# Performance work log

Hardware: AMD Instinct MI355X
Metric: run time of the kernel (lower is better)

The kernel has to match this reference:

```python
import jax, jax.numpy as jnp
import numpy as np
from jax import lax

NMS_THRESH = 0.5      # IoU threshold 'thresh' in the torch forward
MAX_PROPOSALS = 1000  # 'max_proposals' in the torch forward


def setup_inputs() -> dict:
    key = jax.random.key(0)
    k1, k2, k3 = jax.random.split(key, 3)
    N = 10000
    # realistic xyxy boxes inside a ~1000x1000 image
    centers = jax.random.uniform(k1, (N, 2), dtype=jnp.float32) * 1000.0
    wh = jax.random.uniform(k2, (N, 2), dtype=jnp.float32) * 99.0 + 1.0
    boxes = jnp.concatenate([centers - wh / 2.0, centers + wh / 2.0], axis=-1)  # [N,4]
    scores = jax.random.uniform(k3, (N,), dtype=jnp.float32)  # [N]
    return {"boxes": boxes, "scores": scores}


def _pairwise_iou(b):
    # b: [N,4] xyxy, sorted by score. Returns [N,N] IoU matrix.
    x1, y1, x2, y2 = b[:, 0], b[:, 1], b[:, 2], b[:, 3]
    areas = (x2 - x1) * (y2 - y1)                      # [N]
    ix1 = jnp.maximum(x1[:, None], x1[None, :])
    iy1 = jnp.maximum(y1[:, None], y1[None, :])
    ix2 = jnp.minimum(x2[:, None], x2[None, :])
    iy2 = jnp.minimum(y2[:, None], y2[None, :])
    iw = jnp.maximum(ix2 - ix1, 0.0)
    ih = jnp.maximum(iy2 - iy1, 0.0)
    inter = iw * ih                                    # [N,N]
    union = areas[:, None] + areas[None, :] - inter
    return inter / jnp.maximum(union, 1e-9)


def reference(boxes, scores):
    # Faithful greedy NMS: sort by score desc, suppress lower-scored boxes
    # with IoU > thresh against any kept higher-scored box.
    N = boxes.shape[0]
    order = jnp.argsort(-scores)
    b = boxes[order]        # [N,4] score-sorted
    s = scores[order]       # [N]
    ious = _pairwise_iou(b)  # [N,N]
    idx = jnp.arange(N)

    def body(i, keep):
        # if box i is still kept, suppress all later boxes overlapping it
        suppress = keep[i] & (ious[i] > NMS_THRESH) & (idx > i)
        return keep & ~suppress

    keep = lax.fori_loop(0, N, body, jnp.ones((N,), dtype=bool))
    # keep = keep[:max_proposals] in the torch code: first MAX_PROPOSALS kept boxes
    rank = jnp.cumsum(keep.astype(jnp.int32)) - 1
    keep = keep & (rank < MAX_PROPOSALS)
    # fixed-shape equivalent of boxlist[keep]: zero out suppressed entries
    boxes_out = jnp.where(keep[:, None], b, 0.0)   # [N,4]
    scores_out = jnp.where(keep, s, 0.0)           # [N]
    return boxes_out, scores_out, keep
```

## Files before the change

kernel.cpp:

```cpp
#include <hip/hip_runtime.h>
#include <stdint.h>

#define MAX_PROPOSALS 1000
#define WPAD 160
#define NSTRIPE 128
#define SCAP 2048
#define LDSE 13312
#define G 10
#define NCELL (G * G)
#define NB 4096

__device__ __forceinline__ int cell_of(float lo, float hi) {
  int g = (int)((lo + hi) * 0.005f);
  return min(max(g, 0), G - 1);
}
__device__ __forceinline__ int bucket_of(float s) {
  int b = (int)(s * (float)NB);
  return min(max(b, 0), NB - 1);
}

__global__ __launch_bounds__(1024) void k_zero(int* __restrict__ p, int n) {
  for (int i = threadIdx.x; i < n; i += 1024) p[i] = 0;
}

__global__ __launch_bounds__(256) void k_hist(const float* __restrict__ scores,
                                              const float4* __restrict__ boxes,
                                              int* __restrict__ hist,
                                              int* __restrict__ cellCnt, int N) {
  int i = blockIdx.x * 256 + threadIdx.x;
  if (i >= N) return;
  float s = scores[i];
  atomicAdd(&hist[bucket_of(s)], 1);
  float4 b = boxes[i];
  int cell = cell_of(b.y, b.w) * G + cell_of(b.x, b.z);
  atomicAdd(&cellCnt[cell], 1);
}

__global__ __launch_bounds__(1024) void k_prefix(const int* __restrict__ hist,
                       int* __restrict__ bstart, int* __restrict__ bcur,
                       const int* __restrict__ cellCnt,
                       int* __restrict__ cellStart, int* __restrict__ cellCur) {
  __shared__ int wsum[16];
  int tid = threadIdx.x, l = tid & 63, wv = tid >> 6;
  int h[4];
  int base4 = tid * 4;
  int s = 0;
  #pragma unroll
  for (int k = 0; k < 4; ++k) { h[k] = hist[base4 + k]; s += h[k]; }
  int inc = s;
  #pragma unroll
  for (int d = 1; d < 64; d <<= 1) {
    int v = __shfl_up(inc, d, 64);
    if (l >= d) inc += v;
  }
  if (l == 63) wsum[wv] = inc;
  __syncthreads();
  if (tid == 0) {
    int run = 0;
    for (int w = 0; w < 16; ++w) { int v = wsum[w]; wsum[w] = run; run += v; }
  }
  __syncthreads();
  int ex = wsum[wv] + inc - s;
  #pragma unroll
  for (int k = 0; k < 4; ++k) { bstart[base4 + k] = ex; bcur[base4 + k] = ex; ex += h[k]; }
  if (tid == 1023) bstart[NB] = ex;

  if (wv == 0) {
    int a = (2 * l < NCELL) ? cellCnt[2 * l] : 0;
    int b = (2 * l + 1 < NCELL) ? cellCnt[2 * l + 1] : 0;
    int s2 = a + b, inc2 = s2;
    #pragma unroll
    for (int d = 1; d < 64; d <<= 1) {
      int v = __shfl_up(inc2, d, 64);
      if (l >= d) inc2 += v;
    }
    int ex2 = inc2 - s2;
    if (2 * l < NCELL)     { cellStart[2 * l] = ex2;         cellCur[2 * l] = ex2; }
    if (2 * l + 1 < NCELL) { cellStart[2 * l + 1] = ex2 + a; cellCur[2 * l + 1] = ex2 + a; }
    if (l == 63) cellStart[NCELL] = inc2;
  }
}

__global__ __launch_bounds__(256) void k_bscatter(const float* __restrict__ scores,
                       int* __restrict__ bcur, uint64_t* __restrict__ bkey,
                       int* __restrict__ bidx, int N) {
  int i = blockIdx.x * 256 + threadIdx.x;
  if (i >= N) return;
  float s = scores[i];
  uint64_t key = ((uint64_t)__float_as_uint(s) << 32) | (uint64_t)(0xFFFFFFFFu - (uint32_t)i);
  int b = bucket_of(s);
  int pos = atomicAdd(&bcur[b], 1);
  bkey[pos] = key;
  bidx[pos] = i;
}

__global__ __launch_bounds__(256) void k_rankscatter(const uint64_t* __restrict__ bkey,
                       const int* __restrict__ bidx, const int* __restrict__ bstart,
                       const float4* __restrict__ boxes,
                       int* __restrict__ cellCur,
                       float4* __restrict__ sbox, float* __restrict__ ss,
                       float4* __restrict__ sboxC, int* __restrict__ cellRank, int N) {
  int p = blockIdx.x * 256 + threadIdx.x;
  if (p >= N) return;
  uint64_t key = bkey[p];
  float s = __uint_as_float((uint32_t)(key >> 32));
  int b = bucket_of(s);
  int q0 = bstart[b], q1 = bstart[b + 1];
  int r = N - q1;
  for (int q = q0; q < q1; ++q) r += (bkey[q] > key);
  int idx = bidx[p];
  float4 bx = boxes[idx];
  sbox[r] = bx;
  ss[r] = s;
  int cell = cell_of(bx.y, bx.w) * G + cell_of(bx.x, bx.z);
  int cpos = atomicAdd(&cellCur[cell], 1);
  sboxC[cpos] = bx;
  cellRank[cpos] = r;
}

__global__ __launch_bounds__(256) void k_maskR2(const float4* __restrict__ sbox,
                        const int* __restrict__ cellStart,
                        const float4* __restrict__ sboxC, const int* __restrict__ cellRank,
                        uint32_t* __restrict__ edges, int* __restrict__ ecnt, int N) {
  int wv = threadIdx.x >> 6, lane = threadIdx.x & 63;
  int i = blockIdx.x * 4 + wv;
  if (i >= N) return;
  int stripe = blockIdx.x & (NSTRIPE - 1);
  uint32_t* estr = edges + (size_t)stripe * SCAP;

  float4 iB = sbox[i];
  float iar = (iB.z - iB.x) * (iB.w - iB.y);
  int cx = cell_of(iB.x, iB.z), cy = cell_of(iB.y, iB.w);
  int x0 = max(cx - 1, 0), x1 = min(cx + 1, G - 1);
  int y0 = max(cy - 1, 0), y1 = min(cy + 1, G - 1);

  for (int ry = y0; ry <= y1; ++ry) {
    int s = cellStart[ry * G + x0];
    int e = cellStart[ry * G + x1 + 1];
    if (s >= e) continue;

    int p = s + lane;
    int pc = (p < e) ? p : s;
    float4 cB = sboxC[pc];
    int rk = cellRank[pc];

    for (int p0 = s; p0 < e; p0 += 64) {
      float4 curB = cB;
      int currk = rk;
      bool curv = (p0 + lane) < e;

      if (p0 + 64 < e) {
        int np = p0 + 64 + lane;
        int npc = (np < e) ? np : s;
        cB = sboxC[npc];
        rk = cellRank[npc];
      }

      float car = (curB.z - curB.x) * (curB.w - curB.y);
      float ix1 = fmaxf(iB.x, curB.x);
      float iy1 = fmaxf(iB.y, curB.y);
      float ix2 = fminf(iB.z, curB.z);
      float iy2 = fminf(iB.w, curB.w);
      float iw = fmaxf(ix2 - ix1, 0.0f);
      float ih = fmaxf(iy2 - iy1, 0.0f);
      float inter = iw * ih;
      float uni = (iar + car) - inter;
      float m_ = fmaxf(uni, 1e-9f);
      float t_ = 0.5f * m_;
      bool pred = (inter > t_) && curv && (currk > i);
      bool ambig = pred && (inter <= t_ + t_ * 3e-7f);
      if (__builtin_expect(__ballot(ambig) != 0ull, 0)) {
        if (ambig) pred = (inter / m_) > 0.5f;
      }
      uint64_t ball = __ballot(pred);
      if (__builtin_expect(ball != 0ull, 0)) {
        int cnt = __popcll(ball);
        int base = 0;
        if (lane == 0) base = atomicAdd(&ecnt[stripe], cnt);
        base = __shfl(base, 0, 64);
        if (pred) {
          int pos = base + __popcll(ball & ((1ull << lane) - 1ull));
          if (pos < SCAP) estr[pos] = ((uint32_t)i << 14) | (uint32_t)currk;
        }
      }
    }
  }
}

__global__ __launch_bounds__(1024) void k_scanJ(const uint32_t* __restrict__ edges,
                                                const int* __restrict__ ecnt,
                                                uint64_t* __restrict__ keepw,
                                                int* __restrict__ wpref, int N) {
  const int tid = threadIdx.x, l = tid & 63, wave = tid >> 6;
  const int nw = (N + 63) >> 6;
  const int nh = 2 * nw;

  __shared__ uint32_t eL[LDSE];
  __shared__ int scnt[NSTRIPE], soff[NSTRIPE];
  __shared__ int eTot;
  __shared__ uint32_t kc[2 * WPAD];
  __shared__ uint32_t kn[2 * WPAD];
  __shared__ uint32_t baseL[2 * WPAD];
  __shared__ uint64_t keepL[WPAD];
  __shared__ int chgS;

  if (wave == 0) {
    int a = min(ecnt[2 * l], SCAP);
    int b = min(ecnt[2 * l + 1], SCAP);
    int s = a + b, inc = s;
    #pragma unroll
    for (int d = 1; d < 64; d <<= 1) {
      int v = __shfl_up(inc, d, 64);
      if (l >= d) inc += v;
    }
    int ex = inc - s;
    scnt[2 * l] = a;     soff[2 * l] = ex;
    scnt[2 * l + 1] = b; soff[2 * l + 1] = ex + a;
    if (l == 63) eTot = min(inc, LDSE);
  }
  for (int w = tid; w < 2 * WPAD; w += 1024) {
    long lo = (long)(w >> 1) * 64 + (long)(w & 1) * 32;
    long rem = (long)N - lo;
    uint32_t m = (rem >= 32) ? 0xFFFFFFFFu : ((rem <= 0) ? 0u : ((1u << rem) - 1u));
    baseL[w] = m;
    kc[w] = m;
  }
  __syncthreads();

  for (int s = wave; s < NSTRIPE; s += 16) {
    int cnt = scnt[s], off = soff[s];
    const uint32_t* src = edges + (size_t)s * SCAP;
    for (int k = l; k < cnt; k += 64) {
      int dst = off + k;
      if (dst < LDSE) eL[dst] = src[k];
    }
  }
  __syncthreads();
  int EL = eTot;

  for (int round = 0; round < 10001; ++round) {
    for (int w = tid; w < nh; w += 1024) kn[w] = baseL[w];
    if (tid == 0) chgS = 0;
    __syncthreads();

    for (int e = tid; e < EL; e += 1024) {
      uint32_t p = eL[e];
      int i = (int)(p >> 14);
      int j = (int)(p & 0x3FFFu);
      if ((kc[i >> 5] >> (i & 31)) & 1u)
        atomicAnd(&kn[j >> 5], ~(1u << (j & 31)));
    }
    __syncthreads();

    int local = 0;
    for (int w = tid; w < nh; w += 1024) {
      uint32_t a = kn[w];
      if (a != kc[w]) local = 1;
      kc[w] = a;
    }
    if (local) chgS = 1;
    __syncthreads();
    bool done = (chgS == 0);
    __syncthreads();
    if (done) break;
  }

  for (int i = tid; i < WPAD; i += 1024)
    keepL[i] = (i < nw) ? (((uint64_t)kc[2 * i + 1] << 32) | (uint64_t)kc[2 * i]) : 0ull;
  __syncthreads();

  if (wave == 0) {
    uint64_t k0 = keepL[l], k1 = keepL[64 + l];
    uint64_t k2v = (128 + l < WPAD) ? keepL[128 + l] : 0ull;
    int p0 = __popcll(k0), p1 = __popcll(k1), p2 = __popcll(k2v);
    int s0 = p0, s1 = p1, s2 = p2;
    #pragma unroll
    for (int d = 1; d < 64; d <<= 1) {
      int v0 = __shfl_up(s0, d, 64), v1 = __shfl_up(s1, d, 64), v2 = __shfl_up(s2, d, 64);
      if (l >= d) { s0 += v0; s1 += v1; s2 += v2; }
    }
    int tot0 = __shfl(s0, 63, 64);
    int tot1 = __shfl(s1, 63, 64);
    keepw[l] = k0;
    keepw[64 + l] = k1;
    if (128 + l < WPAD) keepw[128 + l] = k2v;
    wpref[l] = s0 - p0;
    wpref[64 + l] = tot0 + s1 - p1;
    if (128 + l < WPAD) wpref[128 + l] = tot0 + tot1 + s2 - p2;
  }
}

__global__ __launch_bounds__(256) void k_out(const float4* __restrict__ sbox,
                      const float* __restrict__ ss,
                      const uint64_t* __restrict__ keepw, const int* __restrict__ wpref,
                      float* __restrict__ out, int N) {
  int i = blockIdx.x * 256 + threadIdx.x;
  if (i >= N) return;
  int w = i >> 6, b = i & 63;
  uint64_t kw = keepw[w];
  bool kept = (kw >> b) & 1ull;
  int rank = wpref[w] + __popcll(kw & ((1ull << b) - 1ull));
  bool fin = kept && (rank < MAX_PROPOSALS);
  float4 bx = sbox[i];
  if (!fin) { bx.x = 0.0f; bx.y = 0.0f; bx.z = 0.0f; bx.w = 0.0f; }
  ((float4*)out)[i] = bx;
  out[(size_t)4 * N + i] = fin ? ss[i] : 0.0f;
  out[(size_t)5 * N + i] = fin ? 1.0f : 0.0f;
}

extern "C" void kernel_launch(void* const* d_in, const int* in_sizes, int n_in,
                              void* d_out, int out_size, void* d_ws, size_t ws_size,
                              hipStream_t stream) {
  const float4* boxes = (const float4*)d_in[0];
  const float* scores = (const float*)d_in[1];
  int N = in_sizes[1];

  char* ws = (char*)d_ws;
  size_t off = 0;
  int* hist    = (int*)(ws + off); off += NB * 4;
  int* ecnt    = (int*)(ws + off); off += NSTRIPE * 4;
  int* cellCnt = (int*)(ws + off); off += NCELL * 4;
  int zints = NB + NSTRIPE + NCELL;
  off = (off + 255) & ~(size_t)255;
  int* bstart   = (int*)(ws + off); off += (NB + 1) * 4;
  int* bcur     = (int*)(ws + off); off += NB * 4;
  int* cellStart= (int*)(ws + off); off += (NCELL + 1) * 4;
  int* cellCur  = (int*)(ws + off); off += NCELL * 4;
  off = (off + 255) & ~(size_t)255;
  uint64_t* bkey = (uint64_t*)(ws + off); off += (size_t)N * 8;
  int* bidx      = (int*)(ws + off); off += (size_t)N * 4;
  off = (off + 255) & ~(size_t)255;
  float4* sbox  = (float4*)(ws + off); off += (size_t)N * 16;
  float4* sboxC = (float4*)(ws + off); off += (size_t)N * 16;
  float* ss     = (float*)(ws + off);  off += (size_t)N * 4;
  int* cellRank = (int*)(ws + off); off += (size_t)N * 4;
  off = (off + 255) & ~(size_t)255;
  uint32_t* edges = (uint32_t*)(ws + off); off += (size_t)NSTRIPE * SCAP * 4;
  uint64_t* keepw = (uint64_t*)(ws + off); off += WPAD * 8;
  int* wpref      = (int*)(ws + off); off += WPAD * 4;

  int nblk = (N + 255) / 256;

  k_zero<<<1, 1024, 0, stream>>>(hist, zints);
  k_hist<<<nblk, 256, 0, stream>>>(scores, boxes, hist, cellCnt, N);
  k_prefix<<<1, 1024, 0, stream>>>(hist, bstart, bcur, cellCnt, cellStart, cellCur);
  k_bscatter<<<nblk, 256, 0, stream>>>(scores, bcur, bkey, bidx, N);
  k_rankscatter<<<nblk, 256, 0, stream>>>(bkey, bidx, bstart, boxes, cellCur,
                                          sbox, ss, sboxC, cellRank, N);
  k_maskR2<<<(N + 3) / 4, 256, 0, stream>>>(sbox, cellStart, sboxC, cellRank, edges, ecnt, N);
  k_scanJ<<<1, 1024, 0, stream>>>(edges, ecnt, keepw, wpref, N);
  k_out<<<nblk, 256, 0, stream>>>(sbox, ss, keepw, wpref, (float*)d_out, N);
}
```

Baseline: 121.6 us.

## Fuse all NMS stages into one cooperative kernel with grid syncs

Replaces eight separate kernel launches with a single cooperative kernel of 256 blocks of 256 threads. Stages are separated by grid.sync() and use grid-stride loops. The goal is to remove per-launch overhead and inter-kernel gaps, which dominate a pipeline of many tiny kernels. The trade-offs: the serial label-propagation stage now runs in one 256-thread block instead of 1024 threads, the mask stage has far fewer waves in flight, and each grid barrier has its own cost.

```diff
diff --git a/kernel.cpp b/kernel.cpp
--- a/kernel.cpp
+++ b/kernel.cpp
@@ -1,5 +1,8 @@
 #include <hip/hip_runtime.h>
+#include <hip/hip_cooperative_groups.h>
 #include <stdint.h>
+
+namespace cg = cooperative_groups;
 
 #define MAX_PROPOSALS 1000
 #define WPAD 160
@@ -9,6 +12,8 @@
 #define G 10
 #define NCELL (G * G)
 #define NB 4096
+#define NBLK 256
+#define NTHR 256
 
 __device__ __forceinline__ int cell_of(float lo, float hi) {
   int g = (int)((lo + hi) * 0.005f);
@@ -19,53 +24,68 @@
   return min(max(b, 0), NB - 1);
 }
 
-__global__ __launch_bounds__(1024) void k_zero(int* __restrict__ p, int n) {
-  for (int i = threadIdx.x; i < n; i += 1024) p[i] = 0;
-}
-
-__global__ __launch_bounds__(256) void k_hist(const float* __restrict__ scores,
-                                              const float4* __restrict__ boxes,
-                                              int* __restrict__ hist,
-                                              int* __restrict__ cellCnt, int N) {
-  int i = blockIdx.x * 256 + threadIdx.x;
-  if (i >= N) return;
-  float s = scores[i];
-  atomicAdd(&hist[bucket_of(s)], 1);
-  float4 b = boxes[i];
-  int cell = cell_of(b.y, b.w) * G + cell_of(b.x, b.z);
-  atomicAdd(&cellCnt[cell], 1);
-}
-
-__global__ __launch_bounds__(1024) void k_prefix(const int* __restrict__ hist,
-                       int* __restrict__ bstart, int* __restrict__ bcur,
-                       const int* __restrict__ cellCnt,
-                       int* __restrict__ cellStart, int* __restrict__ cellCur) {
-  __shared__ int wsum[16];
-  int tid = threadIdx.x, l = tid & 63, wv = tid >> 6;
-  int h[4];
-  int base4 = tid * 4;
-  int s = 0;
-  #pragma unroll
-  for (int k = 0; k < 4; ++k) { h[k] = hist[base4 + k]; s += h[k]; }
-  int inc = s;
-  #pragma unroll
-  for (int d = 1; d < 64; d <<= 1) {
-    int v = __shfl_up(inc, d, 64);
-    if (l >= d) inc += v;
-  }
-  if (l == 63) wsum[wv] = inc;
-  __syncthreads();
-  if (tid == 0) {
-    int run = 0;
-    for (int w = 0; w < 16; ++w) { int v = wsum[w]; wsum[w] = run; run += v; }
-  }
-  __syncthreads();
-  int ex = wsum[wv] + inc - s;
-  #pragma unroll
-  for (int k = 0; k < 4; ++k) { bstart[base4 + k] = ex; bcur[base4 + k] = ex; ex += h[k]; }
-  if (tid == 1023) bstart[NB] = ex;
-
-  if (wv == 0) {
+__global__ __launch_bounds__(NTHR) void k_all(
+    const float4* __restrict__ boxes, const float* __restrict__ scores,
+    int* __restrict__ hist,
+    int* __restrict__ ecnt, int* __restrict__ cellCnt,
+    int* __restrict__ bstart, int* __restrict__ bcur,
+    int* __restrict__ cellStart, int* __restrict__ cellCur,
+    uint64_t* __restrict__ bkey, int* __restrict__ bidx,
+    float4* __restrict__ sbox, float* __restrict__ ss,
+    float4* __restrict__ sboxC, int* __restrict__ cellRank,
+    uint32_t* __restrict__ edges, uint64_t* __restrict__ keepw,
+    int* __restrict__ wpref, float* __restrict__ out, int N) {
+  cg::grid_group grid = cg::this_grid();
+  const int tid = threadIdx.x, bid = blockIdx.x;
+  const int gtid = bid * NTHR + tid;
+  const int P = NBLK * NTHR;
+  const int l = tid & 63, wv = tid >> 6;
+  const int nw = (N + 63) >> 6;
+  const int nh = 2 * nw;
+
+  __shared__ int psum[4];
+  __shared__ uint32_t eL[LDSE];
+  __shared__ int scnt[NSTRIPE], soff[NSTRIPE];
+  __shared__ int eTotS;
+  __shared__ uint32_t kc[2 * WPAD], kn[2 * WPAD], baseL[2 * WPAD];
+  __shared__ uint64_t keepL[WPAD];
+  __shared__ int chgS;
+
+  for (int i = gtid; i < NB + NSTRIPE + NCELL; i += P) hist[i] = 0;
+  grid.sync();
+
+  for (int i = gtid; i < N; i += P) {
+    float s = scores[i];
+    atomicAdd(&hist[bucket_of(s)], 1);
+    float4 b = boxes[i];
+    atomicAdd(&cellCnt[cell_of(b.y, b.w) * G + cell_of(b.x, b.z)], 1);
+  }
+  grid.sync();
+
+  if (bid == 0) {
+    int h[16];
+    int base16 = tid * 16;
+    int s = 0;
+    #pragma unroll
+    for (int k = 0; k < 16; ++k) { h[k] = hist[base16 + k]; s += h[k]; }
+    int inc = s;
+    #pragma unroll
+    for (int d = 1; d < 64; d <<= 1) {
+      int v = __shfl_up(inc, d, 64);
+      if (l >= d) inc += v;
+    }
+    if (l == 63) psum[wv] = inc;
+    __syncthreads();
+    if (tid == 0) {
+      int run = 0;
+      for (int w = 0; w < 4; ++w) { int v = psum[w]; psum[w] = run; run += v; }
+    }
+    __syncthreads();
+    int ex = psum[wv] + inc - s;
+    #pragma unroll
+    for (int k = 0; k < 16; ++k) { bstart[base16 + k] = ex; bcur[base16 + k] = ex; ex += h[k]; }
+    if (tid == NTHR - 1) bstart[NB] = ex;
+  } else if (bid == 1 && wv == 0) {
     int a = (2 * l < NCELL) ? cellCnt[2 * l] : 0;
     int b = (2 * l + 1 < NCELL) ? cellCnt[2 * l + 1] : 0;
     int s2 = a + b, inc2 = s2;
@@ -79,233 +99,191 @@
     if (2 * l + 1 < NCELL) { cellStart[2 * l + 1] = ex2 + a; cellCur[2 * l + 1] = ex2 + a; }
     if (l == 63) cellStart[NCELL] = inc2;
   }
-}
-
-__global__ __launch_bounds__(256) void k_bscatter(const float* __restrict__ scores,
-                       int* __restrict__ bcur, uint64_t* __restrict__ bkey,
-                       int* __restrict__ bidx, int N) {
-  int i = blockIdx.x * 256 + threadIdx.x;
-  if (i >= N) return;
-  float s = scores[i];
-  uint64_t key = ((uint64_t)__float_as_uint(s) << 32) | (uint64_t)(0xFFFFFFFFu - (uint32_t)i);
-  int b = bucket_of(s);
-  int pos = atomicAdd(&bcur[b], 1);
-  bkey[pos] = key;
-  bidx[pos] = i;
-}
-
-__global__ __launch_bounds__(256) void k_rankscatter(const uint64_t* __restrict__ bkey,
-                       const int* __restrict__ bidx, const int* __restrict__ bstart,
-                       const float4* __restrict__ boxes,
-                       int* __restrict__ cellCur,
-                       float4* __restrict__ sbox, float* __restrict__ ss,
-                       float4* __restrict__ sboxC, int* __restrict__ cellRank, int N) {
-  int p = blockIdx.x * 256 + threadIdx.x;
-  if (p >= N) return;
-  uint64_t key = bkey[p];
-  float s = __uint_as_float((uint32_t)(key >> 32));
-  int b = bucket_of(s);
-  int q0 = bstart[b], q1 = bstart[b + 1];
-  int r = N - q1;
-  for (int q = q0; q < q1; ++q) r += (bkey[q] > key);
-  int idx = bidx[p];
-  float4 bx = boxes[idx];
-  sbox[r] = bx;
-  ss[r] = s;
-  int cell = cell_of(bx.y, bx.w) * G + cell_of(bx.x, bx.z);
-  int cpos = atomicAdd(&cellCur[cell], 1);
-  sboxC[cpos] = bx;
-  cellRank[cpos] = r;
-}
-
-__global__ __launch_bounds__(256) void k_maskR2(const float4* __restrict__ sbox,
-                        const int* __restrict__ cellStart,
-                        const float4* __restrict__ sboxC, const int* __restrict__ cellRank,
-                        uint32_t* __restrict__ edges, int* __restrict__ ecnt, int N) {
-  int wv = threadIdx.x >> 6, lane = threadIdx.x & 63;
-  int i = blockIdx.x * 4 + wv;
-  if (i >= N) return;
-  int stripe = blockIdx.x & (NSTRIPE - 1);
-  uint32_t* estr = edges + (size_t)stripe * SCAP;
-
-  float4 iB = sbox[i];
-  float iar = (iB.z - iB.x) * (iB.w - iB.y);
-  int cx = cell_of(iB.x, iB.z), cy = cell_of(iB.y, iB.w);
-  int x0 = max(cx - 1, 0), x1 = min(cx + 1, G - 1);
-  int y0 = max(cy - 1, 0), y1 = min(cy + 1, G - 1);
-
-  for (int ry = y0; ry <= y1; ++ry) {
-    int s = cellStart[ry * G + x0];
-    int e = cellStart[ry * G + x1 + 1];
-    if (s >= e) continue;
-
-    int p = s + lane;
-    int pc = (p < e) ? p : s;
-    float4 cB = sboxC[pc];
-    int rk = cellRank[pc];
-
-    for (int p0 = s; p0 < e; p0 += 64) {
-      float4 curB = cB;
-      int currk = rk;
-      bool curv = (p0 + lane) < e;
-
-      if (p0 + 64 < e) {
-        int np = p0 + 64 + lane;
-        int npc = (np < e) ? np : s;
-        cB = sboxC[npc];
-        rk = cellRank[npc];
-      }
-
-      float car = (curB.z - curB.x) * (curB.w - curB.y);
-      float ix1 = fmaxf(iB.x, curB.x);
-      float iy1 = fmaxf(iB.y, curB.y);
-      float ix2 = fminf(iB.z, curB.z);
-      float iy2 = fminf(iB.w, curB.w);
-      float iw = fmaxf(ix2 - ix1, 0.0f);
-      float ih = fmaxf(iy2 - iy1, 0.0f);
-      float inter = iw * ih;
-      float uni = (iar + car) - inter;
-      float m_ = fmaxf(uni, 1e-9f);
-      float t_ = 0.5f * m_;
-      bool pred = (inter > t_) && curv && (currk > i);
-      bool ambig = pred && (inter <= t_ + t_ * 3e-7f);
-      if (__builtin_expect(__ballot(ambig) != 0ull, 0)) {
-        if (ambig) pred = (inter / m_) > 0.5f;
-      }
-      uint64_t ball = __ballot(pred);
-      if (__builtin_expect(ball != 0ull, 0)) {
-        int cnt = __popcll(ball);
-        int base = 0;
-        if (lane == 0) base = atomicAdd(&ecnt[stripe], cnt);
-        base = __shfl(base, 0, 64);
-        if (pred) {
-          int pos = base + __popcll(ball & ((1ull << lane) - 1ull));
-          if (pos < SCAP) estr[pos] = ((uint32_t)i << 14) | (uint32_t)currk;
+  grid.sync();
+
+  for (int i = gtid; i < N; i += P) {
+    float s = scores[i];
+    uint64_t key = ((uint64_t)__float_as_uint(s) << 32) | (uint64_t)(0xFFFFFFFFu - (uint32_t)i);
+    int pos = atomicAdd(&bcur[bucket_of(s)], 1);
+    bkey[pos] = key;
+    bidx[pos] = i;
+  }
+  grid.sync();
+
+  for (int p = gtid; p < N; p += P) {
+    uint64_t key = bkey[p];
+    float s = __uint_as_float((uint32_t)(key >> 32));
+    int b = bucket_of(s);
+    int q0 = bstart[b], q1 = bstart[b + 1];
+    int r = N - q1;
+    for (int q = q0; q < q1; ++q) r += (bkey[q] > key);
+    float4 bx = boxes[bidx[p]];
+    sbox[r] = bx;
+    ss[r] = s;
+    int cpos = atomicAdd(&cellCur[cell_of(bx.y, bx.w) * G + cell_of(bx.x, bx.z)], 1);
+    sboxC[cpos] = bx;
+    cellRank[cpos] = r;
+  }
+  grid.sync();
+
+  {
+    int wvid = (bid << 2) | wv;
+    for (int i = wvid; i < N; i += NBLK * 4) {
+      int stripe = i & (NSTRIPE - 1);
+      uint32_t* estr = edges + (size_t)stripe * SCAP;
+      float4 iB = sbox[i];
+      float iar = (iB.z - iB.x) * (iB.w - iB.y);
+      int cx = cell_of(iB.x, iB.z), cy = cell_of(iB.y, iB.w);
+      int x0 = max(cx - 1, 0), x1 = min(cx + 1, G - 1);
+      int y0 = max(cy - 1, 0), y1 = min(cy + 1, G - 1);
+
+      for (int ry = y0; ry <= y1; ++ry) {
+        int s = cellStart[ry * G + x0];
+        int e = cellStart[ry * G + x1 + 1];
+        if (s >= e) continue;
+        int p = s + l;
+        int pc = (p < e) ? p : s;
+        float4 cB = sboxC[pc];
+        int rk = cellRank[pc];
+        for (int p0 = s; p0 < e; p0 += 64) {
+          float4 curB = cB;
+          int currk = rk;
+          bool curv = (p0 + l) < e;
+          if (p0 + 64 < e) {
+            int np = p0 + 64 + l;
+            int npc = (np < e) ? np : s;
+            cB = sboxC[npc];
+            rk = cellRank[npc];
+          }
+          float car = (curB.z - curB.x) * (curB.w - curB.y);
+          float ix1 = fmaxf(iB.x, curB.x);
+          float iy1 = fmaxf(iB.y, curB.y);
+          float ix2 = fminf(iB.z, curB.z);
+          float iy2 = fminf(iB.w, curB.w);
+          float iw = fmaxf(ix2 - ix1, 0.0f);
+          float ih = fmaxf(iy2 - iy1, 0.0f);
+          float inter = iw * ih;
+          float uni = (iar + car) - inter;
+          float m_ = fmaxf(uni, 1e-9f);
+          float t_ = 0.5f * m_;
+          bool pred = (inter > t_) && curv && (currk > i);
+          bool ambig = pred && (inter <= t_ + t_ * 3e-7f);
+          if (__builtin_expect(__ballot(ambig) != 0ull, 0)) {
+            if (ambig) pred = (inter / m_) > 0.5f;
+          }
+          uint64_t ball = __ballot(pred);
+          if (__builtin_expect(ball != 0ull, 0)) {
+            int cnt = __popcll(ball);
+            int base = 0;
+            if (l == 0) base = atomicAdd(&ecnt[stripe], cnt);
+            base = __shfl(base, 0, 64);
+            if (pred) {
+              int pos = base + __popcll(ball & ((1ull << l) - 1ull));
+              if (pos < SCAP) estr[pos] = ((uint32_t)i << 14) | (uint32_t)currk;
+            }
+          }
         }
       }
     }
   }
-}
-
-__global__ __launch_bounds__(1024) void k_scanJ(const uint32_t* __restrict__ edges,
-                                                const int* __restrict__ ecnt,
-                                                uint64_t* __restrict__ keepw,
-                                                int* __restrict__ wpref, int N) {
-  const int tid = threadIdx.x, l = tid & 63, wave = tid >> 6;
-  const int nw = (N + 63) >> 6;
-  const int nh = 2 * nw;
-
-  __shared__ uint32_t eL[LDSE];
-  __shared__ int scnt[NSTRIPE], soff[NSTRIPE];
-  __shared__ int eTot;
-  __shared__ uint32_t kc[2 * WPAD];
-  __shared__ uint32_t kn[2 * WPAD];
-  __shared__ uint32_t baseL[2 * WPAD];
-  __shared__ uint64_t keepL[WPAD];
-  __shared__ int chgS;
-
-  if (wave == 0) {
-    int a = min(ecnt[2 * l], SCAP);
-    int b = min(ecnt[2 * l + 1], SCAP);
-    int s = a + b, inc = s;
-    #pragma unroll
-    for (int d = 1; d < 64; d <<= 1) {
-      int v = __shfl_up(inc, d, 64);
-      if (l >= d) inc += v;
-    }
-    int ex = inc - s;
-    scnt[2 * l] = a;     soff[2 * l] = ex;
-    scnt[2 * l + 1] = b; soff[2 * l + 1] = ex + a;
-    if (l == 63) eTot = min(inc, LDSE);
-  }
-  for (int w = tid; w < 2 * WPAD; w += 1024) {
-    long lo = (long)(w >> 1) * 64 + (long)(w & 1) * 32;
-    long rem = (long)N - lo;
-    uint32_t m = (rem >= 32) ? 0xFFFFFFFFu : ((rem <= 0) ? 0u : ((1u << rem) - 1u));
-    baseL[w] = m;
-    kc[w] = m;
-  }
-  __syncthreads();
-
-  for (int s = wave; s < NSTRIPE; s += 16) {
-    int cnt = scnt[s], off = soff[s];
-    const uint32_t* src = edges + (size_t)s * SCAP;
-    for (int k = l; k < cnt; k += 64) {
-      int dst = off + k;
-      if (dst < LDSE) eL[dst] = src[k];
-    }
-  }
-  __syncthreads();
-  int EL = eTot;
-
-  for (int round = 0; round < 10001; ++round) {
-    for (int w = tid; w < nh; w += 1024) kn[w] = baseL[w];
-    if (tid == 0) chgS = 0;
-    __syncthreads();
-
-    for (int e = tid; e < EL; e += 1024) {
-      uint32_t p = eL[e];
-      int i = (int)(p >> 14);
-      int j = (int)(p & 0x3FFFu);
-      if ((kc[i >> 5] >> (i & 31)) & 1u)
-        atomicAnd(&kn[j >> 5], ~(1u << (j & 31)));
-    }
-    __syncthreads();
-
-    int local = 0;
-    for (int w = tid; w < nh; w += 1024) {
-      uint32_t a = kn[w];
-      if (a != kc[w]) local = 1;
-      kc[w] = a;
-    }
-    if (local) chgS = 1;
-    __syncthreads();
-    bool done = (chgS == 0);
-    __syncthreads();
-    if (done) break;
-  }
-
-  for (int i = tid; i < WPAD; i += 1024)
-    keepL[i] = (i < nw) ? (((uint64_t)kc[2 * i + 1] << 32) | (uint64_t)kc[2 * i]) : 0ull;
-  __syncthreads();
-
-  if (wave == 0) {
-    uint64_t k0 = keepL[l], k1 = keepL[64 + l];
-    uint64_t k2v = (128 + l < WPAD) ? keepL[128 + l] : 0ull;
-    int p0 = __popcll(k0), p1 = __popcll(k1), p2 = __popcll(k2v);
-    int s0 = p0, s1 = p1, s2 = p2;
-    #pragma unroll
-    for (int d = 1; d < 64; d <<= 1) {
-      int v0 = __shfl_up(s0, d, 64), v1 = __shfl_up(s1, d, 64), v2 = __shfl_up(s2, d, 64);
-      if (l >= d) { s0 += v0; s1 += v1; s2 += v2; }
-    }
-    int tot0 = __shfl(s0, 63, 64);
-    int tot1 = __shfl(s1, 63, 64);
-    keepw[l] = k0;
-    keepw[64 + l] = k1;
-    if (128 + l < WPAD) keepw[128 + l] = k2v;
-    wpref[l] = s0 - p0;
-    wpref[64 + l] = tot0 + s1 - p1;
-    if (128 + l < WPAD) wpref[128 + l] = tot0 + tot1 + s2 - p2;
-  }
-}
-
-__global__ __launch_bounds__(256) void k_out(const float4* __restrict__ sbox,
-                      const float* __restrict__ ss,
-                      const uint64_t* __restrict__ keepw, const int* __restrict__ wpref,
-                      float* __restrict__ out, int N) {
-  int i = blockIdx.x * 256 + threadIdx.x;
-  if (i >= N) return;
-  int w = i >> 6, b = i & 63;
-  uint64_t kw = keepw[w];
-  bool kept = (kw >> b) & 1ull;
-  int rank = wpref[w] + __popcll(kw & ((1ull << b) - 1ull));
-  bool fin = kept && (rank < MAX_PROPOSALS);
-  float4 bx = sbox[i];
-  if (!fin) { bx.x = 0.0f; bx.y = 0.0f; bx.z = 0.0f; bx.w = 0.0f; }
-  ((float4*)out)[i] = bx;
-  out[(size_t)4 * N + i] = fin ? ss[i] : 0.0f;
-  out[(size_t)5 * N + i] = fin ? 1.0f : 0.0f;
+  grid.sync();
+
+  if (bid == 0) {
+    if (wv == 0) {
+      int a = min(ecnt[2 * l], SCAP);
+      int b = min(ecnt[2 * l + 1], SCAP);
+      int s = a + b, inc = s;
+      #pragma unroll
+      for (int d = 1; d < 64; d <<= 1) {
+        int v = __shfl_up(inc, d, 64);
+        if (l >= d) inc += v;
+      }
+      int ex = inc - s;
+      scnt[2 * l] = a;     soff[2 * l] = ex;
+      scnt[2 * l + 1] = b; soff[2 * l + 1] = ex + a;
+      if (l == 63) eTotS = min(inc, LDSE);
+    }
+    for (int w = tid; w < 2 * WPAD; w += NTHR) {
+      long lo = (long)(w >> 1) * 64 + (long)(w & 1) * 32;
+      long rem = (long)N - lo;
+      uint32_t m = (rem >= 32) ? 0xFFFFFFFFu : ((rem <= 0) ? 0u : ((1u << rem) - 1u));
+      baseL[w] = m;
+      kc[w] = m;
+    }
+    __syncthreads();
+    for (int s = wv; s < NSTRIPE; s += 4) {
+      int cnt = scnt[s], off = soff[s];
+      const uint32_t* src = edges + (size_t)s * SCAP;
+      for (int k = l; k < cnt; k += 64) {
+        int dst = off + k;
+        if (dst < LDSE) eL[dst] = src[k];
+      }
+    }
+    __syncthreads();
+    int EL = eTotS;
+
+    for (int round = 0; round < 10001; ++round) {
+      for (int w = tid; w < nh; w += NTHR) kn[w] = baseL[w];
+      if (tid == 0) chgS = 0;
+      __syncthreads();
+      for (int e = tid; e < EL; e += NTHR) {
+        uint32_t p = eL[e];
+        int i = (int)(p >> 14);
+        int j = (int)(p & 0x3FFFu);
+        if ((kc[i >> 5] >> (i & 31)) & 1u)
+          atomicAnd(&kn[j >> 5], ~(1u << (j & 31)));
+      }
+      __syncthreads();
+      int local = 0;
+      for (int w = tid; w < nh; w += NTHR) {
+        uint32_t a = kn[w];
+        if (a != kc[w]) local = 1;
+        kc[w] = a;
+      }
+      if (local) chgS = 1;
+      __syncthreads();
+      bool done = (chgS == 0);
+      __syncthreads();
+      if (done) break;
+    }
+
+    for (int i = tid; i < WPAD; i += NTHR)
+      keepL[i] = (i < nw) ? (((uint64_t)kc[2 * i + 1] << 32) | (uint64_t)kc[2 * i]) : 0ull;
+    __syncthreads();
+    if (wv == 0) {
+      uint64_t k0 = keepL[l], k1 = keepL[64 + l];
+      uint64_t k2v = (128 + l < WPAD) ? keepL[128 + l] : 0ull;
+      int p0 = __popcll(k0), p1 = __popcll(k1), p2 = __popcll(k2v);
+      int s0 = p0, s1 = p1, s2 = p2;
+      #pragma unroll
+      for (int d = 1; d < 64; d <<= 1) {
+        int v0 = __shfl_up(s0, d, 64), v1 = __shfl_up(s1, d, 64), v2 = __shfl_up(s2, d, 64);
+        if (l >= d) { s0 += v0; s1 += v1; s2 += v2; }
+      }
+      int tot0 = __shfl(s0, 63, 64);
+      int tot1 = __shfl(s1, 63, 64);
+      keepw[l] = k0;
+      keepw[64 + l] = k1;
+      if (128 + l < WPAD) keepw[128 + l] = k2v;
+      wpref[l] = s0 - p0;
+      wpref[64 + l] = tot0 + s1 - p1;
+      if (128 + l < WPAD) wpref[128 + l] = tot0 + tot1 + s2 - p2;
+    }
+  }
+  grid.sync();
+
+  for (int i = gtid; i < N; i += P) {
+    int w = i >> 6, b = i & 63;
+    uint64_t kw = keepw[w];
+    bool kept = (kw >> b) & 1ull;
+    int rank = wpref[w] + __popcll(kw & ((1ull << b) - 1ull));
+    bool fin = kept && (rank < MAX_PROPOSALS);
+    float4 bx = sbox[i];
+    if (!fin) { bx.x = 0.0f; bx.y = 0.0f; bx.z = 0.0f; bx.w = 0.0f; }
+    ((float4*)out)[i] = bx;
+    out[(size_t)4 * N + i] = fin ? ss[i] : 0.0f;
+    out[(size_t)5 * N + i] = fin ? 1.0f : 0.0f;
+  }
 }
 
 extern "C" void kernel_launch(void* const* d_in, const int* in_sizes, int n_in,
@@ -320,12 +298,11 @@
   int* hist    = (int*)(ws + off); off += NB * 4;
   int* ecnt    = (int*)(ws + off); off += NSTRIPE * 4;
   int* cellCnt = (int*)(ws + off); off += NCELL * 4;
-  int zints = NB + NSTRIPE + NCELL;
   off = (off + 255) & ~(size_t)255;
-  int* bstart   = (int*)(ws + off); off += (NB + 1) * 4;
-  int* bcur     = (int*)(ws + off); off += NB * 4;
-  int* cellStart= (int*)(ws + off); off += (NCELL + 1) * 4;
-  int* cellCur  = (int*)(ws + off); off += NCELL * 4;
+  int* bstart    = (int*)(ws + off); off += (NB + 1) * 4;
+  int* bcur      = (int*)(ws + off); off += NB * 4;
+  int* cellStart = (int*)(ws + off); off += (NCELL + 1) * 4;
+  int* cellCur   = (int*)(ws + off); off += NCELL * 4;
   off = (off + 255) & ~(size_t)255;
   uint64_t* bkey = (uint64_t*)(ws + off); off += (size_t)N * 8;
   int* bidx      = (int*)(ws + off); off += (size_t)N * 4;
@@ -339,15 +316,15 @@
   uint64_t* keepw = (uint64_t*)(ws + off); off += WPAD * 8;
   int* wpref      = (int*)(ws + off); off += WPAD * 4;
 
-  int nblk = (N + 255) / 256;
-
-  k_zero<<<1, 1024, 0, stream>>>(hist, zints);
-  k_hist<<<nblk, 256, 0, stream>>>(scores, boxes, hist, cellCnt, N);
-  k_prefix<<<1, 1024, 0, stream>>>(hist, bstart, bcur, cellCnt, cellStart, cellCur);
-  k_bscatter<<<nblk, 256, 0, stream>>>(scores, bcur, bkey, bidx, N);
-  k_rankscatter<<<nblk, 256, 0, stream>>>(bkey, bidx, bstart, boxes, cellCur,
-                                          sbox, ss, sboxC, cellRank, N);
-  k_maskR2<<<(N + 3) / 4, 256, 0, stream>>>(sbox, cellStart, sboxC, cellRank, edges, ecnt, N);
-  k_scanJ<<<1, 1024, 0, stream>>>(edges, ecnt, keepw, wpref, N);
-  k_out<<<nblk, 256, 0, stream>>>(sbox, ss, keepw, wpref, (float*)d_out, N);
+  float* outp = (float*)d_out;
+  void* args[] = {
+    (void*)&boxes, (void*)&scores,
+    (void*)&hist, (void*)&ecnt, (void*)&cellCnt,
+    (void*)&bstart, (void*)&bcur, (void*)&cellStart, (void*)&cellCur,
+    (void*)&bkey, (void*)&bidx,
+    (void*)&sbox, (void*)&ss, (void*)&sboxC, (void*)&cellRank,
+    (void*)&edges, (void*)&keepw, (void*)&wpref,
+    (void*)&outp, (void*)&N,
+  };
+  hipLaunchCooperativeKernel((void*)k_all, dim3(NBLK), dim3(NTHR), args, 0, stream);
 }
```

Result: slower. 325.3 us (+167.5%).

## Remove zero and output kernels via per-block histograms and fused output

Applied to the files above, without the earlier changes.

The zeroing kernel is eliminated: the histogram now builds per-block LDS histograms and writes them to a 2D buffer, which the prefix kernel reduces. The prefix kernel also zeroes the edge counters. The output kernel is folded into the single-block scan kernel, which writes the final boxes, scores and keep flags directly from LDS keep bits. This cuts two kernel launches and removes global atomics, but the output now runs in one block of 1024 threads, and the prefix kernel does serial reads across up to 10 partial histograms.

```diff
diff --git a/kernel.cpp b/kernel.cpp
--- a/kernel.cpp
+++ b/kernel.cpp
@@ -9,6 +9,7 @@
 #define G 10
 #define NCELL (G * G)
 #define NB 4096
+#define NHBMAX 16
 
 __device__ __forceinline__ int cell_of(float lo, float hi) {
   int g = (int)((lo + hi) * 0.005f);
@@ -19,34 +20,45 @@
   return min(max(b, 0), NB - 1);
 }
 
-__global__ __launch_bounds__(1024) void k_zero(int* __restrict__ p, int n) {
-  for (int i = threadIdx.x; i < n; i += 1024) p[i] = 0;
-}
-
-__global__ __launch_bounds__(256) void k_hist(const float* __restrict__ scores,
-                                              const float4* __restrict__ boxes,
-                                              int* __restrict__ hist,
-                                              int* __restrict__ cellCnt, int N) {
-  int i = blockIdx.x * 256 + threadIdx.x;
-  if (i >= N) return;
-  float s = scores[i];
-  atomicAdd(&hist[bucket_of(s)], 1);
-  float4 b = boxes[i];
-  int cell = cell_of(b.y, b.w) * G + cell_of(b.x, b.z);
-  atomicAdd(&cellCnt[cell], 1);
-}
-
-__global__ __launch_bounds__(1024) void k_prefix(const int* __restrict__ hist,
+__global__ __launch_bounds__(1024) void k_hist(const float* __restrict__ scores,
+                                               const float4* __restrict__ boxes,
+                                               int* __restrict__ hist2d,
+                                               int* __restrict__ cell2d, int N) {
+  __shared__ int lh[NB];
+  __shared__ int lc[NCELL];
+  int tid = threadIdx.x, b = blockIdx.x;
+  for (int k = tid; k < NB; k += 1024) lh[k] = 0;
+  if (tid < NCELL) lc[tid] = 0;
+  __syncthreads();
+  int i = b * 1024 + tid;
+  if (i < N) {
+    atomicAdd(&lh[bucket_of(scores[i])], 1);
+    float4 bx = boxes[i];
+    atomicAdd(&lc[cell_of(bx.y, bx.w) * G + cell_of(bx.x, bx.z)], 1);
+  }
+  __syncthreads();
+  for (int k = tid; k < NB; k += 1024) hist2d[(size_t)b * NB + k] = lh[k];
+  if (tid < NCELL) cell2d[b * NCELL + tid] = lc[tid];
+}
+
+__global__ __launch_bounds__(1024) void k_prefix(const int* __restrict__ hist2d,
+                       const int* __restrict__ cell2d, int nhb,
                        int* __restrict__ bstart, int* __restrict__ bcur,
-                       const int* __restrict__ cellCnt,
-                       int* __restrict__ cellStart, int* __restrict__ cellCur) {
+                       int* __restrict__ cellStart, int* __restrict__ cellCur,
+                       int* __restrict__ ecnt) {
   __shared__ int wsum[16];
   int tid = threadIdx.x, l = tid & 63, wv = tid >> 6;
+  if (tid < NSTRIPE) ecnt[tid] = 0;
+
   int h[4];
   int base4 = tid * 4;
   int s = 0;
   #pragma unroll
-  for (int k = 0; k < 4; ++k) { h[k] = hist[base4 + k]; s += h[k]; }
+  for (int k = 0; k < 4; ++k) {
+    int v = 0;
+    for (int c = 0; c < nhb; ++c) v += hist2d[(size_t)c * NB + base4 + k];
+    h[k] = v; s += v;
+  }
   int inc = s;
   #pragma unroll
   for (int d = 1; d < 64; d <<= 1) {
@@ -66,8 +78,9 @@
   if (tid == 1023) bstart[NB] = ex;
 
   if (wv == 0) {
-    int a = (2 * l < NCELL) ? cellCnt[2 * l] : 0;
-    int b = (2 * l + 1 < NCELL) ? cellCnt[2 * l + 1] : 0;
+    int a = 0, b = 0;
+    if (2 * l < NCELL)     for (int c = 0; c < nhb; ++c) a += cell2d[c * NCELL + 2 * l];
+    if (2 * l + 1 < NCELL) for (int c = 0; c < nhb; ++c) b += cell2d[c * NCELL + 2 * l + 1];
     int s2 = a + b, inc2 = s2;
     #pragma unroll
     for (int d = 1; d < 64; d <<= 1) {
@@ -189,8 +202,9 @@
 
 __global__ __launch_bounds__(1024) void k_scanJ(const uint32_t* __restrict__ edges,
                                                 const int* __restrict__ ecnt,
-                                                uint64_t* __restrict__ keepw,
-                                                int* __restrict__ wpref, int N) {
+                                                const float4* __restrict__ sbox,
+                                                const float* __restrict__ ss,
+                                                float* __restrict__ out, int N) {
   const int tid = threadIdx.x, l = tid & 63, wave = tid >> 6;
   const int nw = (N + 63) >> 6;
   const int nh = 2 * nw;
@@ -202,6 +216,7 @@
   __shared__ uint32_t kn[2 * WPAD];
   __shared__ uint32_t baseL[2 * WPAD];
   __shared__ uint64_t keepL[WPAD];
+  __shared__ int wprefL[WPAD];
   __shared__ int chgS;
 
   if (wave == 0) {
@@ -281,31 +296,27 @@
     }
     int tot0 = __shfl(s0, 63, 64);
     int tot1 = __shfl(s1, 63, 64);
-    keepw[l] = k0;
-    keepw[64 + l] = k1;
-    if (128 + l < WPAD) keepw[128 + l] = k2v;
-    wpref[l] = s0 - p0;
-    wpref[64 + l] = tot0 + s1 - p1;
-    if (128 + l < WPAD) wpref[128 + l] = tot0 + tot1 + s2 - p2;
-  }
-}
-
-__global__ __launch_bounds__(256) void k_out(const float4* __restrict__ sbox,
-                      const float* __restrict__ ss,
-                      const uint64_t* __restrict__ keepw, const int* __restrict__ wpref,
-                      float* __restrict__ out, int N) {
-  int i = blockIdx.x * 256 + threadIdx.x;
-  if (i >= N) return;
-  int w = i >> 6, b = i & 63;
-  uint64_t kw = keepw[w];
-  bool kept = (kw >> b) & 1ull;
-  int rank = wpref[w] + __popcll(kw & ((1ull << b) - 1ull));
-  bool fin = kept && (rank < MAX_PROPOSALS);
-  float4 bx = sbox[i];
-  if (!fin) { bx.x = 0.0f; bx.y = 0.0f; bx.z = 0.0f; bx.w = 0.0f; }
-  ((float4*)out)[i] = bx;
-  out[(size_t)4 * N + i] = fin ? ss[i] : 0.0f;
-  out[(size_t)5 * N + i] = fin ? 1.0f : 0.0f;
+    wprefL[l] = s0 - p0;
+    wprefL[64 + l] = tot0 + s1 - p1;
+    if (128 + l < WPAD) wprefL[128 + l] = tot0 + tot1 + s2 - p2;
+  }
+  __syncthreads();
+
+  float4* bo = (float4*)out;
+  float* so = out + (size_t)4 * N;
+  float* ko = so + N;
+  for (int i = tid; i < N; i += 1024) {
+    int w = i >> 6, b = i & 63;
+    uint64_t kwv = keepL[w];
+    bool kept = (kwv >> b) & 1ull;
+    int rank = wprefL[w] + __popcll(kwv & ((1ull << b) - 1ull));
+    bool fin = kept && (rank < MAX_PROPOSALS);
+    float4 bx = sbox[i];
+    if (!fin) { bx.x = 0.0f; bx.y = 0.0f; bx.z = 0.0f; bx.w = 0.0f; }
+    bo[i] = bx;
+    so[i] = fin ? ss[i] : 0.0f;
+    ko[i] = fin ? 1.0f : 0.0f;
+  }
 }
 
 extern "C" void kernel_launch(void* const* d_in, const int* in_sizes, int n_in,
@@ -314,13 +325,14 @@
   const float4* boxes = (const float4*)d_in[0];
   const float* scores = (const float*)d_in[1];
   int N = in_sizes[1];
+  int nhb = (N + 1023) / 1024;
+  if (nhb > NHBMAX) nhb = NHBMAX;
 
   char* ws = (char*)d_ws;
   size_t off = 0;
-  int* hist    = (int*)(ws + off); off += NB * 4;
-  int* ecnt    = (int*)(ws + off); off += NSTRIPE * 4;
-  int* cellCnt = (int*)(ws + off); off += NCELL * 4;
-  int zints = NB + NSTRIPE + NCELL;
+  int* hist2d = (int*)(ws + off); off += (size_t)NHBMAX * NB * 4;
+  int* cell2d = (int*)(ws + off); off += (size_t)NHBMAX * NCELL * 4;
+  int* ecnt   = (int*)(ws + off); off += NSTRIPE * 4;
   off = (off + 255) & ~(size_t)255;
   int* bstart   = (int*)(ws + off); off += (NB + 1) * 4;
   int* bcur     = (int*)(ws + off); off += NB * 4;
@@ -336,18 +348,15 @@
   int* cellRank = (int*)(ws + off); off += (size_t)N * 4;
   off = (off + 255) & ~(size_t)255;
   uint32_t* edges = (uint32_t*)(ws + off); off += (size_t)NSTRIPE * SCAP * 4;
-  uint64_t* keepw = (uint64_t*)(ws + off); off += WPAD * 8;
-  int* wpref      = (int*)(ws + off); off += WPAD * 4;
 
   int nblk = (N + 255) / 256;
 
-  k_zero<<<1, 1024, 0, stream>>>(hist, zints);
-  k_hist<<<nblk, 256, 0, stream>>>(scores, boxes, hist, cellCnt, N);
-  k_prefix<<<1, 1024, 0, stream>>>(hist, bstart, bcur, cellCnt, cellStart, cellCur);
+  k_hist<<<nhb, 1024, 0, stream>>>(scores, boxes, hist2d, cell2d, N);
+  k_prefix<<<1, 1024, 0, stream>>>(hist2d, cell2d, nhb, bstart, bcur,
+                                   cellStart, cellCur, ecnt);
   k_bscatter<<<nblk, 256, 0, stream>>>(scores, bcur, bkey, bidx, N);
   k_rankscatter<<<nblk, 256, 0, stream>>>(bkey, bidx, bstart, boxes, cellCur,
                                           sbox, ss, sboxC, cellRank, N);
   k_maskR2<<<(N + 3) / 4, 256, 0, stream>>>(sbox, cellStart, sboxC, cellRank, edges, ecnt, N);
-  k_scanJ<<<1, 1024, 0, stream>>>(edges, ecnt, keepw, wpref, N);
-  k_out<<<nblk, 256, 0, stream>>>(sbox, ss, keepw, wpref, (float*)d_out, N);
-}
+  k_scanJ<<<1, 1024, 0, stream>>>(edges, ecnt, sbox, ss, (float*)d_out, N);
+}
```

New measurement: 122.2 us. About the same (+0.5%).
